# Performance work log

Hardware: AMD Instinct MI355X
Metric: run time of the kernel (lower is better)

## Reference

```python
import jax, jax.numpy as jnp
import numpy as np

B, I, O = 512, 1024, 1024

def setup_inputs() -> dict:
    key = jax.random.key(0)
    kx, kw = jax.random.split(key)
    x = jax.random.normal(kx, (B, I), dtype=jnp.float32)
    W = jax.random.normal(kw, (O, I), dtype=jnp.float32)
    return {"x": x, "W": W}

def reference(x, W):
    # Tropical (max-plus) linear map: y[b, o] = max_i (x[b, i] + W[o, i])
    # Faithful to the torch broadcast-add + max-reduce formulation.
    out = x[..., None, :] + W[None, :, :]  # [B, O, I]
    return jnp.max(out, axis=-1)           # [B, O]
```

## Files before the change

kernel.cpp:

```cpp
#include <hip/hip_runtime.h>
#include <float.h>


#define B_DIM 512
#define I_DIM 1024
#define O_DIM 1024
#define BT 128
#define OT 128
#define KT 32

static_assert(sizeof(float4) == 16, "");

__device__ __forceinline__ void g2lds16(const float* g, float* l) {
    __builtin_amdgcn_global_load_lds(
        (const __attribute__((address_space(1))) void*)g,
        (__attribute__((address_space(3))) void*)l, 16, 0, 0);
}

template <int KB>
__global__ __launch_bounds__(256, 1) void trop_main(
    const float* __restrict__ x,
    const float* __restrict__ W,
    float* __restrict__ part)
{
    constexpr int NCH = KB / KT;
    __shared__ float xs[2][BT * KT];
    __shared__ float ws[2][OT * KT];

    const int tid  = threadIdx.x;
    const int to   = tid & 15;
    const int tb   = tid >> 4;
    const int wave = tid >> 6;
    const int lane = tid & 63;
    const int o0 = blockIdx.x * OT;
    const int b0 = blockIdx.y * BT;
    const int kz = blockIdx.z;
    const int kbase = kz * KB;

    const int ro8 = lane >> 3;
    const int q   = (lane & 7) ^ ro8;

    float acc[8][8];
    #pragma unroll
    for (int i = 0; i < 8; ++i)
        #pragma unroll
        for (int j = 0; j < 8; ++j)
            acc[i][j] = -FLT_MAX;

    auto stage = [&](int c, int buf) {
        const int k0 = kbase + c * KT;
        #pragma unroll
        for (int i = 0; i < 4; ++i) {
            const int t = wave * 4 + i;
            g2lds16(&x[(size_t)(b0 + 8 * t + ro8) * I_DIM + k0 + 4 * q],
                    &xs[buf][t * 256]);
        }
        #pragma unroll
        for (int i = 0; i < 4; ++i) {
            const int t = wave * 4 + i;
            g2lds16(&W[(size_t)(o0 + 8 * t + ro8) * I_DIM + k0 + 4 * q],
                    &ws[buf][t * 256]);
        }
    };

    const int swx = tb & 7;
    const int swo = to & 7;

    auto compute = [&](int buf) {
        #pragma unroll 2
        for (int kq = 0; kq < KT / 4; ++kq) {
            float4 xv[8], wv[8];
            #pragma unroll
            for (int ii = 0; ii < 8; ++ii)
                xv[ii] = *(const float4*)&xs[buf][(tb + 16 * ii) * KT + 4 * (kq ^ swx)];
            #pragma unroll
            for (int jj = 0; jj < 8; ++jj)
                wv[jj] = *(const float4*)&ws[buf][(to + 16 * jj) * KT + 4 * (kq ^ swo)];
            #pragma unroll
            for (int ii = 0; ii < 8; ++ii)
                #pragma unroll
                for (int jj = 0; jj < 8; ++jj) {
                    const float s0 = xv[ii].x + wv[jj].x;
                    const float s1 = xv[ii].y + wv[jj].y;
                    acc[ii][jj] = fmaxf(acc[ii][jj], fmaxf(s0, s1));
                    const float s2 = xv[ii].z + wv[jj].z;
                    const float s3 = xv[ii].w + wv[jj].w;
                    acc[ii][jj] = fmaxf(acc[ii][jj], fmaxf(s2, s3));
                }
        }
    };

    stage(0, 0);
    for (int c = 0; c < NCH; ++c) {
        __syncthreads();
        if (c + 1 < NCH) stage(c + 1, (c + 1) & 1);
        compute(c & 1);
    }

    float* pout = part + (size_t)kz * (B_DIM * O_DIM);
    #pragma unroll
    for (int ii = 0; ii < 8; ++ii) {
        const int b = b0 + tb + 16 * ii;
        #pragma unroll
        for (int jj = 0; jj < 8; ++jj)
            pout[(size_t)b * O_DIM + o0 + to + 16 * jj] = acc[ii][jj];
    }
}

template <int KS>
__global__ __launch_bounds__(256) void trop_reduce(
    const float* __restrict__ part, float* __restrict__ y)
{
    constexpr int N4 = B_DIM * O_DIM / 4;
    const int idx = blockIdx.x * 256 + threadIdx.x;
    const float4* p = (const float4*)part;
    float4 m = p[idx];
    #pragma unroll
    for (int s = 1; s < KS; ++s) {
        const float4 v = p[(size_t)s * N4 + idx];
        m.x = fmaxf(m.x, v.x); m.y = fmaxf(m.y, v.y);
        m.z = fmaxf(m.z, v.z); m.w = fmaxf(m.w, v.w);
    }
    ((float4*)y)[idx] = m;
}

extern "C" void kernel_launch(void* const* d_in, const int* in_sizes, int n_in,
                              void* d_out, int out_size, void* d_ws, size_t ws_size,
                              hipStream_t stream) {
    const float* x = (const float*)d_in[0];
    const float* W = (const float*)d_in[1];
    float* y = (float*)d_out;
    float* part = (float*)d_ws;
    const size_t slab = (size_t)B_DIM * O_DIM * sizeof(float);

    if (ws_size >= 8 * slab) {
        trop_main<I_DIM / 8><<<dim3(O_DIM / OT, B_DIM / BT, 8), 256, 0, stream>>>(x, W, part);
        trop_reduce<8><<<dim3(B_DIM * O_DIM / 4 / 256), 256, 0, stream>>>(part, y);
    } else if (ws_size >= 4 * slab) {
        trop_main<I_DIM / 4><<<dim3(O_DIM / OT, B_DIM / BT, 4), 256, 0, stream>>>(x, W, part);
        trop_reduce<4><<<dim3(B_DIM * O_DIM / 4 / 256), 256, 0, stream>>>(part, y);
    } else if (ws_size >= 2 * slab) {
        trop_main<I_DIM / 2><<<dim3(O_DIM / OT, B_DIM / BT, 2), 256, 0, stream>>>(x, W, part);
        trop_reduce<2><<<dim3(B_DIM * O_DIM / 4 / 256), 256, 0, stream>>>(part, y);
    } else {
        trop_main<I_DIM><<<dim3(O_DIM / OT, B_DIM / BT, 1), 256, 0, stream>>>(x, W, y);
    }
}
```

Measured before the change: 99.06 us.

## Software-pipeline LDS reads in tropical kernel and add 16-way K split

The compute loop is restructured to register double-buffer the x fragments and rotate two W fragments, so LDS loads for the next step are issued while the current add/max chain runs. Launch bounds now allow two blocks per CU. A 16-way K-split path is added when the workspace is large enough. The costs are higher register pressure under the tighter launch bound, and more partial traffic for the reduce kernel if the 16-way path is taken.

```diff
diff --git a/kernel.cpp b/kernel.cpp
--- a/kernel.cpp
+++ b/kernel.cpp
@@ -9,7 +9,7 @@
 #define OT 128
 #define KT 32
 
-static_assert(sizeof(float4) == 16, "");
+typedef float f32x4 __attribute__((ext_vector_type(4)));
 
 __device__ __forceinline__ void g2lds16(const float* g, float* l) {
     __builtin_amdgcn_global_load_lds(
@@ -18,14 +18,16 @@
 }
 
 template <int KB>
-__global__ __launch_bounds__(256, 1) void trop_main(
+__global__ __launch_bounds__(256, 2) void trop_main(
     const float* __restrict__ x,
     const float* __restrict__ W,
     float* __restrict__ part)
 {
     constexpr int NCH = KB / KT;
-    __shared__ float xs[2][BT * KT];
-    __shared__ float ws[2][OT * KT];
+    constexpr int NKQ = KT / 4;
+    static_assert(KB % KT == 0, "");
+    __shared__ __align__(16) float xs[2][BT * KT];
+    __shared__ __align__(16) float ws[2][OT * KT];
 
     const int tid  = threadIdx.x;
     const int to   = tid & 15;
@@ -67,26 +69,46 @@
     const int swo = to & 7;
 
     auto compute = [&](int buf) {
-        #pragma unroll 2
-        for (int kq = 0; kq < KT / 4; ++kq) {
-            float4 xv[8], wv[8];
+        const float* xB = &xs[buf][tb * KT];
+        const float* wB = &ws[buf][to * KT];
+
+        f32x4 xv[2][8];
+        f32x4 wb2[2];
+
+        #pragma unroll
+        for (int ii = 0; ii < 8; ++ii)
+            xv[0][ii] = *(const f32x4*)&xB[ii * 16 * KT + 4 * swx];
+        wb2[0] = *(const f32x4*)&wB[0 * 16 * KT + 4 * swo];
+        wb2[1] = *(const f32x4*)&wB[1 * 16 * KT + 4 * swo];
+
+        #pragma unroll
+        for (int kq = 0; kq < NKQ; ++kq) {
+            const int cur   = kq & 1;
+            const int woff  = 4 * (kq ^ swo);
+            const int xoffN = 4 * ((kq + 1) ^ swx);
+            const int woffN = 4 * ((kq + 1) ^ swo);
+
             #pragma unroll
-            for (int ii = 0; ii < 8; ++ii)
-                xv[ii] = *(const float4*)&xs[buf][(tb + 16 * ii) * KT + 4 * (kq ^ swx)];
-            #pragma unroll
-            for (int jj = 0; jj < 8; ++jj)
-                wv[jj] = *(const float4*)&ws[buf][(to + 16 * jj) * KT + 4 * (kq ^ swo)];
-            #pragma unroll
-            for (int ii = 0; ii < 8; ++ii)
+            for (int jj = 0; jj < 8; ++jj) {
+                const f32x4 wc = wb2[jj & 1];
+                if (jj < 6) {
+                    wb2[jj & 1] = *(const f32x4*)&wB[(jj + 2) * 16 * KT + woff];
+                } else if (kq + 1 < NKQ) {
+                    wb2[jj & 1] = *(const f32x4*)&wB[(jj - 6) * 16 * KT + woffN];
+                    #pragma unroll
+                    for (int u = 0; u < 4; ++u)
+                        xv[cur ^ 1][4 * (jj - 6) + u] =
+                            *(const f32x4*)&xB[(4 * (jj - 6) + u) * 16 * KT + xoffN];
+                }
                 #pragma unroll
-                for (int jj = 0; jj < 8; ++jj) {
-                    const float s0 = xv[ii].x + wv[jj].x;
-                    const float s1 = xv[ii].y + wv[jj].y;
-                    acc[ii][jj] = fmaxf(acc[ii][jj], fmaxf(s0, s1));
-                    const float s2 = xv[ii].z + wv[jj].z;
-                    const float s3 = xv[ii].w + wv[jj].w;
-                    acc[ii][jj] = fmaxf(acc[ii][jj], fmaxf(s2, s3));
+                for (int ii = 0; ii < 8; ++ii) {
+                    const f32x4 s = xv[cur][ii] + wc;
+                    float a = acc[ii][jj];
+                    a = fmaxf(a, fmaxf(s.x, s.y));
+                    a = fmaxf(a, fmaxf(s.z, s.w));
+                    acc[ii][jj] = a;
                 }
+            }
         }
     };
 
@@ -132,16 +154,20 @@
     float* y = (float*)d_out;
     float* part = (float*)d_ws;
     const size_t slab = (size_t)B_DIM * O_DIM * sizeof(float);
+    const dim3 rgrid(B_DIM * O_DIM / 4 / 256);
 
-    if (ws_size >= 8 * slab) {
+    if (ws_size >= 16 * slab) {
+        trop_main<I_DIM / 16><<<dim3(O_DIM / OT, B_DIM / BT, 16), 256, 0, stream>>>(x, W, part);
+        trop_reduce<16><<<rgrid, 256, 0, stream>>>(part, y);
+    } else if (ws_size >= 8 * slab) {
         trop_main<I_DIM / 8><<<dim3(O_DIM / OT, B_DIM / BT, 8), 256, 0, stream>>>(x, W, part);
-        trop_reduce<8><<<dim3(B_DIM * O_DIM / 4 / 256), 256, 0, stream>>>(part, y);
+        trop_reduce<8><<<rgrid, 256, 0, stream>>>(part, y);
     } else if (ws_size >= 4 * slab) {
         trop_main<I_DIM / 4><<<dim3(O_DIM / OT, B_DIM / BT, 4), 256, 0, stream>>>(x, W, part);
-        trop_reduce<4><<<dim3(B_DIM * O_DIM / 4 / 256), 256, 0, stream>>>(part, y);
+        trop_reduce<4><<<rgrid, 256, 0, stream>>>(part, y);
     } else if (ws_size >= 2 * slab) {
         trop_main<I_DIM / 2><<<dim3(O_DIM / OT, B_DIM / BT, 2), 256, 0, stream>>>(x, W, part);
-        trop_reduce<2><<<dim3(B_DIM * O_DIM / 4 / 256), 256, 0, stream>>>(part, y);
+        trop_reduce<2><<<rgrid, 256, 0, stream>>>(part, y);
     } else {
         trop_main<I_DIM><<<dim3(O_DIM / OT, B_DIM / BT, 1), 256, 0, stream>>>(x, W, y);
     }
```

Result: faster. 91.16 us (-8.0%).

## Transpose inputs to k-major layout and vectorize max-plus inner loop

Applied to the files above, without the earlier changes.

Adds transpose kernels that write x and W in k-major order to workspace, so the main kernel loads contiguous rows along b/o into LDS and reads float4 vectors of outputs per k step. The inner loop now broadcasts one x scalar against a vector of W values, with vector stores for results. It also raises the occupancy hint to 2 blocks per CU and the split-K factor to 16 when the workspace allows. The cost is two extra transpose launches and a larger partial-result reduction, plus a naive fallback path.

```diff
diff --git a/kernel.cpp b/kernel.cpp
--- a/kernel.cpp
+++ b/kernel.cpp
@@ -9,7 +9,7 @@
 #define OT 128
 #define KT 32
 
-static_assert(sizeof(float4) == 16, "");
+typedef float f32x4 __attribute__((ext_vector_type(4)));
 
 __device__ __forceinline__ void g2lds16(const float* g, float* l) {
     __builtin_amdgcn_global_load_lds(
@@ -18,14 +18,15 @@
 }
 
 template <int KB>
-__global__ __launch_bounds__(256, 1) void trop_main(
-    const float* __restrict__ x,
-    const float* __restrict__ W,
+__global__ __launch_bounds__(256, 2) void trop_main(
+    const float* __restrict__ xT,
+    const float* __restrict__ wT,
     float* __restrict__ part)
 {
     constexpr int NCH = KB / KT;
-    __shared__ float xs[2][BT * KT];
-    __shared__ float ws[2][OT * KT];
+    static_assert(KB % KT == 0, "");
+    __shared__ __align__(16) float xs[2][KT * BT];
+    __shared__ __align__(16) float ws[2][KT * OT];
 
     const int tid  = threadIdx.x;
     const int to   = tid & 15;
@@ -37,60 +38,68 @@
     const int kz = blockIdx.z;
     const int kbase = kz * KB;
 
-    const int ro8 = lane >> 3;
-    const int q   = (lane & 7) ^ ro8;
-
-    float acc[8][8];
-    #pragma unroll
-    for (int i = 0; i < 8; ++i)
-        #pragma unroll
-        for (int j = 0; j < 8; ++j)
-            acc[i][j] = -FLT_MAX;
+    const int rk = lane >> 5;
+    const int cb = (lane & 31) * 4;
+
+    f32x4 acc[8][2];
+    #pragma unroll
+    for (int i = 0; i < 8; ++i) {
+        acc[i][0] = (f32x4)(-FLT_MAX);
+        acc[i][1] = (f32x4)(-FLT_MAX);
+    }
 
     auto stage = [&](int c, int buf) {
         const int k0 = kbase + c * KT;
         #pragma unroll
         for (int i = 0; i < 4; ++i) {
             const int t = wave * 4 + i;
-            g2lds16(&x[(size_t)(b0 + 8 * t + ro8) * I_DIM + k0 + 4 * q],
+            g2lds16(&xT[(size_t)(k0 + 2 * t + rk) * B_DIM + b0 + cb],
                     &xs[buf][t * 256]);
         }
         #pragma unroll
         for (int i = 0; i < 4; ++i) {
             const int t = wave * 4 + i;
-            g2lds16(&W[(size_t)(o0 + 8 * t + ro8) * I_DIM + k0 + 4 * q],
+            g2lds16(&wT[(size_t)(k0 + 2 * t + rk) * O_DIM + o0 + cb],
                     &ws[buf][t * 256]);
         }
     };
 
-    const int swx = tb & 7;
-    const int swo = to & 7;
-
     auto compute = [&](int buf) {
-        #pragma unroll 2
-        for (int kq = 0; kq < KT / 4; ++kq) {
-            float4 xv[8], wv[8];
+        const float* xB = &xs[buf][4 * tb];
+        const float* wB = &ws[buf][4 * to];
+        #pragma unroll
+        for (int k = 0; k < KT; k += 2) {
+            const f32x4 xa[2] = { *(const f32x4*)&xB[k * BT],
+                                  *(const f32x4*)&xB[k * BT + 64] };
+            const f32x4 xb[2] = { *(const f32x4*)&xB[(k + 1) * BT],
+                                  *(const f32x4*)&xB[(k + 1) * BT + 64] };
+            const f32x4 wa[2] = { *(const f32x4*)&wB[k * OT],
+                                  *(const f32x4*)&wB[k * OT + 64] };
+            const f32x4 wb[2] = { *(const f32x4*)&wB[(k + 1) * OT],
+                                  *(const f32x4*)&wB[(k + 1) * OT + 64] };
             #pragma unroll
-            for (int ii = 0; ii < 8; ++ii)
-                xv[ii] = *(const float4*)&xs[buf][(tb + 16 * ii) * KT + 4 * (kq ^ swx)];
-            #pragma unroll
-            for (int jj = 0; jj < 8; ++jj)
-                wv[jj] = *(const float4*)&ws[buf][(to + 16 * jj) * KT + 4 * (kq ^ swo)];
-            #pragma unroll
-            for (int ii = 0; ii < 8; ++ii)
+            for (int g = 0; g < 2; ++g)
                 #pragma unroll
-                for (int jj = 0; jj < 8; ++jj) {
-                    const float s0 = xv[ii].x + wv[jj].x;
-                    const float s1 = xv[ii].y + wv[jj].y;
-                    acc[ii][jj] = fmaxf(acc[ii][jj], fmaxf(s0, s1));
-                    const float s2 = xv[ii].z + wv[jj].z;
-                    const float s3 = xv[ii].w + wv[jj].w;
-                    acc[ii][jj] = fmaxf(acc[ii][jj], fmaxf(s2, s3));
+                for (int u = 0; u < 4; ++u) {
+                    const float x0 = xa[g][u];
+                    const float x1 = xb[g][u];
+                    #pragma unroll
+                    for (int h = 0; h < 2; ++h) {
+                        const f32x4 s0 = wa[h] + x0;
+                        const f32x4 s1 = wb[h] + x1;
+                        f32x4 a = acc[g * 4 + u][h];
+                        a.x = fmaxf(a.x, fmaxf(s0.x, s1.x));
+                        a.y = fmaxf(a.y, fmaxf(s0.y, s1.y));
+                        a.z = fmaxf(a.z, fmaxf(s0.z, s1.z));
+                        a.w = fmaxf(a.w, fmaxf(s0.w, s1.w));
+                        acc[g * 4 + u][h] = a;
+                    }
                 }
         }
     };
 
     stage(0, 0);
+    #pragma unroll
     for (int c = 0; c < NCH; ++c) {
         __syncthreads();
         if (c + 1 < NCH) stage(c + 1, (c + 1) & 1);
@@ -99,12 +108,32 @@
 
     float* pout = part + (size_t)kz * (B_DIM * O_DIM);
     #pragma unroll
-    for (int ii = 0; ii < 8; ++ii) {
-        const int b = b0 + tb + 16 * ii;
-        #pragma unroll
-        for (int jj = 0; jj < 8; ++jj)
-            pout[(size_t)b * O_DIM + o0 + to + 16 * jj] = acc[ii][jj];
-    }
+    for (int g = 0; g < 2; ++g)
+        #pragma unroll
+        for (int u = 0; u < 4; ++u) {
+            const int b = b0 + 64 * g + 4 * tb + u;
+            #pragma unroll
+            for (int h = 0; h < 2; ++h)
+                *(f32x4*)&pout[(size_t)b * O_DIM + o0 + 64 * h + 4 * to] =
+                    acc[g * 4 + u][h];
+        }
+}
+
+__global__ __launch_bounds__(256) void transpose_k(
+    const float* __restrict__ in, float* __restrict__ out, int R, int C)
+{
+    __shared__ float tile[32][33];
+    const int tx = threadIdx.x;
+    const int ty = threadIdx.y;
+    const int r0 = blockIdx.y * 32;
+    const int c0 = blockIdx.x * 32;
+    #pragma unroll
+    for (int i = 0; i < 4; ++i)
+        tile[ty + 8 * i][tx] = in[(size_t)(r0 + ty + 8 * i) * C + c0 + tx];
+    __syncthreads();
+    #pragma unroll
+    for (int i = 0; i < 4; ++i)
+        out[(size_t)(c0 + ty + 8 * i) * R + r0 + tx] = tile[tx][ty + 8 * i];
 }
 
 template <int KS>
@@ -122,6 +151,18 @@
         m.z = fmaxf(m.z, v.z); m.w = fmaxf(m.w, v.w);
     }
     ((float4*)y)[idx] = m;
+}
+
+__global__ __launch_bounds__(256) void trop_naive(
+    const float* __restrict__ x, const float* __restrict__ W,
+    float* __restrict__ y)
+{
+    const int idx = blockIdx.x * 256 + threadIdx.x;
+    const int b = idx / O_DIM, o = idx % O_DIM;
+    float m = -FLT_MAX;
+    for (int i = 0; i < I_DIM; ++i)
+        m = fmaxf(m, x[b * I_DIM + i] + W[o * I_DIM + i]);
+    y[idx] = m;
 }
 
 extern "C" void kernel_launch(void* const* d_in, const int* in_sizes, int n_in,
@@ -130,19 +171,41 @@
     const float* x = (const float*)d_in[0];
     const float* W = (const float*)d_in[1];
     float* y = (float*)d_out;
-    float* part = (float*)d_ws;
-    const size_t slab = (size_t)B_DIM * O_DIM * sizeof(float);
-
-    if (ws_size >= 8 * slab) {
-        trop_main<I_DIM / 8><<<dim3(O_DIM / OT, B_DIM / BT, 8), 256, 0, stream>>>(x, W, part);
-        trop_reduce<8><<<dim3(B_DIM * O_DIM / 4 / 256), 256, 0, stream>>>(part, y);
-    } else if (ws_size >= 4 * slab) {
-        trop_main<I_DIM / 4><<<dim3(O_DIM / OT, B_DIM / BT, 4), 256, 0, stream>>>(x, W, part);
-        trop_reduce<4><<<dim3(B_DIM * O_DIM / 4 / 256), 256, 0, stream>>>(part, y);
-    } else if (ws_size >= 2 * slab) {
-        trop_main<I_DIM / 2><<<dim3(O_DIM / OT, B_DIM / BT, 2), 256, 0, stream>>>(x, W, part);
-        trop_reduce<2><<<dim3(B_DIM * O_DIM / 4 / 256), 256, 0, stream>>>(part, y);
+
+    const size_t slab  = (size_t)B_DIM * O_DIM * sizeof(float);
+    const size_t xT_sz = (size_t)B_DIM * I_DIM * sizeof(float);
+    const size_t wT_sz = (size_t)O_DIM * I_DIM * sizeof(float);
+    const dim3 rgrid(B_DIM * O_DIM / 4 / 256);
+
+    auto run = [&](auto kmain, int ksplit, float* part, float* xT, float* wT) {
+        transpose_k<<<dim3(I_DIM / 32, B_DIM / 32), dim3(32, 8), 0, stream>>>(x, xT, B_DIM, I_DIM);
+        transpose_k<<<dim3(I_DIM / 32, O_DIM / 32), dim3(32, 8), 0, stream>>>(W, wT, O_DIM, I_DIM);
+        kmain(dim3(O_DIM / OT, B_DIM / BT, ksplit), xT, wT, part);
+    };
+
+    if (ws_size >= 16 * slab + xT_sz + wT_sz) {
+        float* part = (float*)d_ws;
+        float* xT = part + 16 * (B_DIM * O_DIM);
+        float* wT = xT + B_DIM * I_DIM;
+        run([&](dim3 g, const float* a, const float* b, float* p) {
+                trop_main<I_DIM / 16><<<g, 256, 0, stream>>>(a, b, p); },
+            16, part, xT, wT);
+        trop_reduce<16><<<rgrid, 256, 0, stream>>>(part, y);
+    } else if (ws_size >= 8 * slab + xT_sz + wT_sz) {
+        float* part = (float*)d_ws;
+        float* xT = part + 8 * (B_DIM * O_DIM);
+        float* wT = xT + B_DIM * I_DIM;
+        run([&](dim3 g, const float* a, const float* b, float* p) {
+                trop_main<I_DIM / 8><<<g, 256, 0, stream>>>(a, b, p); },
+            8, part, xT, wT);
+        trop_reduce<8><<<rgrid, 256, 0, stream>>>(part, y);
+    } else if (ws_size >= xT_sz + wT_sz) {
+        float* xT = (float*)d_ws;
+        float* wT = xT + B_DIM * I_DIM;
+        run([&](dim3 g, const float* a, const float* b, float* p) {
+                trop_main<I_DIM><<<g, 256, 0, stream>>>(a, b, p); },
+            1, y, xT, wT);
     } else {
-        trop_main<I_DIM><<<dim3(O_DIM / OT, B_DIM / BT, 1), 256, 0, stream>>>(x, W, y);
-    }
-}
+        trop_naive<<<dim3(B_DIM * O_DIM / 256), 256, 0, stream>>>(x, W, y);
+    }
+}
```

New measurement: 371.3 us. 275% more time.
